# Kernel tuning notes

Measured on AMD Instinct MI355X. Metric: run time of the kernel, lower is better.

The kernel has to match this reference:

```python
import jax, jax.numpy as jnp
import numpy as np

HIDDEN = 1024
QKV = 1024
HEADS = 16
HEAD_DIM = QKV // HEADS
B, S = 4, 4096


def setup_inputs() -> dict:
    key = jax.random.key(0)
    ks = jax.random.split(key, 8)
    s = 1.0 / np.sqrt(HIDDEN)
    return {
        "x": jax.random.normal(ks[0], (B, S, HIDDEN), dtype=jnp.float32),
        "mask": jnp.ones((B, S, 1), dtype=jnp.float32),
        "Wq": jax.random.uniform(ks[1], (HIDDEN, QKV), jnp.float32, -s, s),
        "bq": jax.random.uniform(ks[2], (QKV,), jnp.float32, -s, s),
        "Wk": jax.random.uniform(ks[3], (HIDDEN, QKV), jnp.float32, -s, s),
        "bk": jax.random.uniform(ks[4], (QKV,), jnp.float32, -s, s),
        "Wv": jax.random.uniform(ks[5], (HIDDEN, QKV), jnp.float32, -s, s),
        "bv": jax.random.uniform(ks[6], (QKV,), jnp.float32, -s, s),
    }


def _split_heads(t):
    # [B, S, QKV] -> [B, H, S, D]
    b, s, _ = t.shape
    return t.reshape(b, s, HEADS, HEAD_DIM).transpose(0, 2, 1, 3)


def reference(x, mask, Wq, bq, Wk, bk, Wv, bv):
    q = (x @ Wq + bq) * mask  # [B, S, QKV]
    k = (x @ Wk + bk) * mask
    v = (x @ Wv + bv) * mask
    q, k, v = _split_heads(q), _split_heads(k), _split_heads(v)  # [B,H,S,D]
    # k^T @ v : [B, H, D, D]
    kv = jnp.einsum('bhsd,bhse->bhde', k, v)
    # per-batch norm constant from mask sum
    norm = mask.sum(axis=(-1, -2))  # [B]
    norm = 1.0 / jnp.sqrt(norm * HEAD_DIM)
    kv = kv * norm[:, None, None, None]
    # dropout is identity in eval mode
    out = jnp.einsum('bhsd,bhde->bhse', q, kv)  # [B, H, S, D]
    out = out.transpose(0, 2, 1, 3).reshape(B, S, QKV)
    return out
```

## Files before the change

kernel.cpp:

```cpp
#include <hip/hip_runtime.h>
#include <stdint.h>

#define HIDDEN 1024
#define SEQ 4096
#define BATCH 4
#define HEADS 16
#define HDIM 64
#define M_TOT (BATCH * SEQ)
#define NCH 4
#define NT64 16

typedef __bf16 bf16x8 __attribute__((ext_vector_type(8)));
typedef float f32x4 __attribute__((ext_vector_type(4)));
typedef unsigned short u16x8 __attribute__((ext_vector_type(8)));

static __device__ __forceinline__ unsigned short f2bf(float f) {
  union { float f; uint32_t u; } v; v.f = f;
  uint32_t u = v.u;
  uint32_t r = (u + 0x7fffu + ((u >> 16) & 1u)) >> 16;
  return (unsigned short)r;
}
static __device__ __forceinline__ void load_lds16(const void* g, void* l) {
  __builtin_amdgcn_global_load_lds(
      (__attribute__((address_space(1))) void*)(g),
      (__attribute__((address_space(3))) void*)(l), 16, 0, 0);
}

__global__ __launch_bounds__(256) void prep_k(
    const float* __restrict__ x, unsigned short* __restrict__ xb,
    const float* __restrict__ Wk, const float* __restrict__ Wv,
    const float* __restrict__ Wq,
    unsigned short* __restrict__ Bt, unsigned short* __restrict__ Wqt,
    const float* __restrict__ bk, const float* __restrict__ bv,
    float* __restrict__ bkv,
    const float* __restrict__ mask, float* __restrict__ norm) {
  const int bid = blockIdx.x;
  const int tid = threadIdx.x;
  __shared__ float ts[64][65];
  if (bid < 8192) {
    int idx = bid * 256 + tid;
    const float4* xv = (const float4*)x;
    float4 a = xv[(size_t)idx * 2];
    float4 b = xv[(size_t)idx * 2 + 1];
    u16x8 o;
    o[0] = f2bf(a.x); o[1] = f2bf(a.y); o[2] = f2bf(a.z); o[3] = f2bf(a.w);
    o[4] = f2bf(b.x); o[5] = f2bf(b.y); o[6] = f2bf(b.z); o[7] = f2bf(b.w);
    *(u16x8*)(xb + (size_t)idx * 8) = o;
  } else if (bid < 8960) {
    int idx = bid - 8192;
    int z = idx >> 8, rem = idx & 255;
    const float* W = (z == 0) ? Wk : (z == 1) ? Wv : Wq;
    unsigned short* out = (z == 2) ? Wqt : (Bt + (size_t)z * HIDDEN * HIDDEN);
    int n0 = (rem & 15) * 64, k0 = (rem >> 4) * 64;
    int c = tid & 63, rq = tid >> 6;
    for (int i = 0; i < 16; ++i) {
      int r = i * 4 + rq;
      ts[r][c] = W[(size_t)(k0 + r) * HIDDEN + n0 + c];
    }
    __syncthreads();
    for (int i = 0; i < 16; ++i) {
      int n = i * 4 + rq;
      out[(size_t)(n0 + n) * HIDDEN + k0 + c] = f2bf(ts[c][n]);
    }
  } else if (bid < 8968) {
    int i = (bid - 8960) * 256 + tid;
    bkv[i] = (i < HIDDEN) ? bk[i] : bv[i - HIDDEN];
  } else {
    int b = bid - 8968;
    float s = 0.f;
    for (int i = tid; i < SEQ; i += 256) s += mask[b * SEQ + i];
    for (int off = 32; off; off >>= 1) s += __shfl_down(s, off);
    __shared__ float wsum[4];
    if ((tid & 63) == 0) wsum[tid >> 6] = s;
    __syncthreads();
    if (tid == 0) {
      float t = wsum[0] + wsum[1] + wsum[2] + wsum[3];
      norm[b] = rsqrtf(t * (float)HDIM);
    }
  }
}

template <int OUT_MODE>
__global__ __launch_bounds__(512, 2) void gemm256_k(
    const unsigned short* __restrict__ A, const unsigned short* __restrict__ Bt,
    const float* __restrict__ bias, const float* __restrict__ mask,
    void* __restrict__ C, int nbn) {
  __shared__ unsigned short smem[65536];

  const int nwg = gridDim.x;
  const int bid = blockIdx.x;
  const int wg = (bid & 7) * (nwg >> 3) + (bid >> 3);
  const int row0 = (wg / nbn) * 256;
  const int col0 = (wg % nbn) * 256;

  const int tid = threadIdx.x;
  const int wave = tid >> 6;
  const int lane = tid & 63;
  const int wm = wave >> 2;
  const int wn = wave & 3;
  const int lr = lane & 15;
  const int hi = lane >> 4;

  const int srow = tid >> 3;
  const int scol = ((tid & 7) ^ (srow & 7)) * 8;
  const unsigned short* sA = A + (size_t)(row0 + srow) * HIDDEN + scol;
  const unsigned short* sB = Bt + (size_t)(col0 + srow) * HIDDEN + scol;
  const int ldst = tid * 8;

#define STAGE(half, tt, isB) { \
    int dst_ = ((tt)&1) * 32768 + (isB) * 16384 + (half) * 8192 + ldst; \
    const unsigned short* src_ = ((isB) ? sB : sA) + (size_t)(half) * 128 * HIDDEN + (tt) * 64; \
    load_lds16(src_, &smem[dst_]); \
    load_lds16(src_ + (size_t)64 * HIDDEN, &smem[dst_ + 4096]); }

  const int chunk0 = (hi ^ (lr & 7)) * 8;
  const int chunk1 = ((4 + hi) ^ (lr & 7)) * 8;
  const int arow = (wm * 128 + lr) * 64;
  const int brow = 16384 + (wn * 64 + lr) * 64;

  f32x4 acc[8][4];
#pragma unroll
  for (int i = 0; i < 8; ++i)
#pragma unroll
    for (int j = 0; j < 4; ++j) acc[i][j] = (f32x4){0.f, 0.f, 0.f, 0.f};

  STAGE(0, 0, 0) STAGE(1, 0, 0) STAGE(0, 0, 1) STAGE(1, 0, 1)
  STAGE(0, 1, 1) STAGE(1, 1, 1)
  asm volatile("s_waitcnt vmcnt(4)" ::: "memory");
  __builtin_amdgcn_s_barrier();

  bf16x8 af[4][2], b0f[2][2], b1f[2][2];
  for (int t = 0; t < NT64; ++t) {
    const int bb = (t & 1) * 32768;
#pragma unroll
    for (int rf = 0; rf < 4; ++rf) {
      af[rf][0] = *(const bf16x8*)&smem[bb + arow + rf * 1024 + chunk0];
      af[rf][1] = *(const bf16x8*)&smem[bb + arow + rf * 1024 + chunk1];
    }
#pragma unroll
    for (int cf = 0; cf < 2; ++cf) {
      b0f[cf][0] = *(const bf16x8*)&smem[bb + brow + cf * 1024 + chunk0];
      b0f[cf][1] = *(const bf16x8*)&smem[bb + brow + cf * 1024 + chunk1];
    }
    if (t + 1 < NT64) STAGE(0, t + 1, 0)
    __builtin_amdgcn_s_setprio(1);
#pragma unroll
    for (int rf = 0; rf < 4; ++rf)
#pragma unroll
      for (int cf = 0; cf < 2; ++cf)
#pragma unroll
        for (int kh = 0; kh < 2; ++kh)
          acc[rf][cf] = __builtin_amdgcn_mfma_f32_16x16x32_bf16(af[rf][kh], b0f[cf][kh], acc[rf][cf], 0, 0, 0);
    __builtin_amdgcn_s_setprio(0);
    asm volatile("" ::: "memory");
    __builtin_amdgcn_s_barrier();
#pragma unroll
    for (int cf = 0; cf < 2; ++cf) {
      b1f[cf][0] = *(const bf16x8*)&smem[bb + brow + 2048 + cf * 1024 + chunk0];
      b1f[cf][1] = *(const bf16x8*)&smem[bb + brow + 2048 + cf * 1024 + chunk1];
    }
    if (t + 1 < NT64) STAGE(1, t + 1, 0)
    __builtin_amdgcn_s_setprio(1);
#pragma unroll
    for (int rf = 0; rf < 4; ++rf)
#pragma unroll
      for (int cf = 0; cf < 2; ++cf)
#pragma unroll
        for (int kh = 0; kh < 2; ++kh)
          acc[rf][2 + cf] = __builtin_amdgcn_mfma_f32_16x16x32_bf16(af[rf][kh], b1f[cf][kh], acc[rf][2 + cf], 0, 0, 0);
    __builtin_amdgcn_s_setprio(0);
    asm volatile("" ::: "memory");
    __builtin_amdgcn_s_barrier();
#pragma unroll
    for (int rf = 0; rf < 4; ++rf) {
      af[rf][0] = *(const bf16x8*)&smem[bb + arow + 4096 + rf * 1024 + chunk0];
      af[rf][1] = *(const bf16x8*)&smem[bb + arow + 4096 + rf * 1024 + chunk1];
    }
    __builtin_amdgcn_s_setprio(1);
#pragma unroll
    for (int rf = 0; rf < 4; ++rf)
#pragma unroll
      for (int cf = 0; cf < 2; ++cf)
#pragma unroll
        for (int kh = 0; kh < 2; ++kh)
          acc[4 + rf][cf] = __builtin_amdgcn_mfma_f32_16x16x32_bf16(af[rf][kh], b0f[cf][kh], acc[4 + rf][cf], 0, 0, 0);
    __builtin_amdgcn_s_setprio(0);
    asm volatile("" ::: "memory");
    __builtin_amdgcn_s_barrier();
    if (t + 2 < NT64) { STAGE(0, t + 2, 1) STAGE(1, t + 2, 1) }
    __builtin_amdgcn_s_setprio(1);
#pragma unroll
    for (int rf = 0; rf < 4; ++rf)
#pragma unroll
      for (int cf = 0; cf < 2; ++cf)
#pragma unroll
        for (int kh = 0; kh < 2; ++kh)
          acc[4 + rf][2 + cf] = __builtin_amdgcn_mfma_f32_16x16x32_bf16(af[rf][kh], b1f[cf][kh], acc[4 + rf][2 + cf], 0, 0, 0);
    __builtin_amdgcn_s_setprio(0);
    if (t < NT64 - 3) asm volatile("s_waitcnt vmcnt(4)" ::: "memory");
    else              asm volatile("s_waitcnt vmcnt(0)" ::: "memory");
    __builtin_amdgcn_s_barrier();
  }

  float bcol[4];
#pragma unroll
  for (int an = 0; an < 4; ++an)
    bcol[an] = bias[col0 + wn * 64 + (an >> 1) * 32 + (an & 1) * 16 + lr];

  if (OUT_MODE == 2) {
    const int b = row0 >> 12;
    const int s0 = (row0 & 4095) + wm * 128;
    unsigned short* wt = &smem[wave * 4096];
    unsigned short* KVt = (unsigned short*)C;
#pragma unroll
    for (int half = 0; half < 2; ++half) {
#pragma unroll
      for (int am4 = 0; am4 < 4; ++am4) {
#pragma unroll
        for (int j = 0; j < 4; ++j) {
          int r = am4 * 16 + hi * 4 + j;
          float mrow = mask[row0 + wm * 128 + half * 64 + r];
#pragma unroll
          for (int an = 0; an < 4; ++an) {
            int c = (an >> 1) * 32 + (an & 1) * 16 + lr;
            wt[c * 64 + (r ^ ((c & 7) << 3))] =
                f2bf((acc[half * 4 + am4][an][j] + bcol[an]) * mrow);
          }
        }
      }
      asm volatile("s_waitcnt lgkmcnt(0)" ::: "memory");
#pragma unroll
      for (int i = 0; i < 8; ++i) {
        int flat = i * 64 + lane;
        int c = flat >> 3, rq = flat & 7;
        uint4 vv = *(const uint4*)&wt[c * 64 + ((rq * 8) ^ ((c & 7) << 3))];
        *(uint4*)&KVt[((size_t)(col0 + wn * 64 + c) * 4 + b) * 4096 + s0 + half * 64 + rq * 8] = vv;
      }
      asm volatile("s_waitcnt lgkmcnt(0)" ::: "memory");
    }
  } else {
    unsigned short* qv = (unsigned short*)C;
    unsigned short* wt = &smem[wave * 4096];
#pragma unroll
    for (int half = 0; half < 2; ++half) {
#pragma unroll
      for (int am4 = 0; am4 < 4; ++am4) {
#pragma unroll
        for (int j = 0; j < 4; ++j) {
          int r = am4 * 16 + hi * 4 + j;
          float mrow = mask[row0 + wm * 128 + half * 64 + r];
#pragma unroll
          for (int an = 0; an < 4; ++an) {
            int c = (an >> 1) * 32 + (an & 1) * 16 + lr;
            wt[r * 64 + (c ^ ((r & 7) << 3))] =
                f2bf((acc[half * 4 + am4][an][j] + bcol[an]) * mrow);
          }
        }
      }
      asm volatile("s_waitcnt lgkmcnt(0)" ::: "memory");
#pragma unroll
      for (int i = 0; i < 8; ++i) {
        int flat = i * 512 + lane * 8;
        int r = flat >> 6, c0 = flat & 63;
        uint4 vv = *(const uint4*)&wt[r * 64 + (c0 ^ ((r & 7) << 3))];
        *(uint4*)&qv[(size_t)(row0 + wm * 128 + half * 64 + r) * 1024 + col0 + wn * 64 + c0] = vv;
      }
      asm volatile("s_waitcnt lgkmcnt(0)" ::: "memory");
    }
  }
#undef STAGE
}

__global__ __launch_bounds__(256) void kvpart2_k(const unsigned short* __restrict__ KVt,
                                                 float* __restrict__ part) {
  const int bh = blockIdx.x, ch = blockIdx.y;
  const int b = bh >> 4, h = bh & 15;
  __shared__ unsigned short tl[32768];
  const int tid = threadIdx.x;
  const int wave = tid >> 6, lane = tid & 63;
  const int lr = lane & 15, hi = lane >> 4;

  const int r0 = tid >> 3;
  const int cc0 = ((tid & 7) ^ (r0 & 7)) * 8;
  const int r1 = 32 + r0;
  const int cc1 = ((tid & 7) ^ (r1 & 7)) * 8;
  const unsigned short* A0 = KVt + ((size_t)(h * 64 + r0) * 4 + b) * 4096 + ch * 1024 + cc0;
  const unsigned short* A1 = KVt + ((size_t)(h * 64 + r1) * 4 + b) * 4096 + ch * 1024 + cc1;
  const unsigned short* B0 = KVt + ((size_t)(1024 + h * 64 + r0) * 4 + b) * 4096 + ch * 1024 + cc0;
  const unsigned short* B1 = KVt + ((size_t)(1024 + h * 64 + r1) * 4 + b) * 4096 + ch * 1024 + cc1;

#define KSTAGE(tt) { int bb2 = ((tt) & 3) * 8192; \
    load_lds16(A0 + (tt) * 64, &tl[bb2 + tid * 8]); \
    load_lds16(A1 + (tt) * 64, &tl[bb2 + 2048 + tid * 8]); \
    load_lds16(B0 + (tt) * 64, &tl[bb2 + 4096 + tid * 8]); \
    load_lds16(B1 + (tt) * 64, &tl[bb2 + 6144 + tid * 8]); }

  const int ra = wave * 16 + lr;
  const int aoff = ra * 64;
  const int ach0 = (hi ^ (ra & 7)) * 8, ach1 = ((4 + hi) ^ (ra & 7)) * 8;

  f32x4 acc4[4];
#pragma unroll
  for (int nt = 0; nt < 4; ++nt) acc4[nt] = (f32x4){0.f, 0.f, 0.f, 0.f};

  KSTAGE(0) KSTAGE(1)
  asm volatile("s_waitcnt vmcnt(4)" ::: "memory");
  __builtin_amdgcn_s_barrier();
  for (int t = 0; t < 16; ++t) {
    const int bb = (t & 3) * 8192;
    if (t + 2 < 16) KSTAGE(t + 2)
    bf16x8 a0 = *(const bf16x8*)&tl[bb + aoff + ach0];
    bf16x8 a1 = *(const bf16x8*)&tl[bb + aoff + ach1];
    bf16x8 bf0[4], bf1[4];
#pragma unroll
    for (int nt = 0; nt < 4; ++nt) {
      int rb = nt * 16 + lr;
      bf0[nt] = *(const bf16x8*)&tl[bb + 4096 + rb * 64 + ((hi ^ (rb & 7)) * 8)];
      bf1[nt] = *(const bf16x8*)&tl[bb + 4096 + rb * 64 + (((4 + hi) ^ (rb & 7)) * 8)];
    }
#pragma unroll
    for (int nt = 0; nt < 4; ++nt) {
      acc4[nt] = __builtin_amdgcn_mfma_f32_16x16x32_bf16(a0, bf0[nt], acc4[nt], 0, 0, 0);
      acc4[nt] = __builtin_amdgcn_mfma_f32_16x16x32_bf16(a1, bf1[nt], acc4[nt], 0, 0, 0);
    }
    if (t < 14) asm volatile("s_waitcnt vmcnt(4)" ::: "memory");
    else        asm volatile("s_waitcnt vmcnt(0)" ::: "memory");
    __builtin_amdgcn_s_barrier();
  }
  float* dst = part + ((size_t)(ch * 64 + bh)) * 4096;
#pragma unroll
  for (int nt = 0; nt < 4; ++nt)
#pragma unroll
    for (int j = 0; j < 4; ++j)
      dst[(wave * 16 + hi * 4 + j) * 64 + nt * 16 + lr] = acc4[nt][j];
#undef KSTAGE
}

__global__ void kvreduce_k(const float* __restrict__ part, const float* __restrict__ norm,
                           unsigned short* __restrict__ kvt) {
  int idx4 = (blockIdx.x * 256 + threadIdx.x) * 4;
  int bh = idx4 >> 12, rem = idx4 & 4095;
  int e = rem >> 6, d0 = rem & 63;
  float s0 = 0.f, s1 = 0.f, s2 = 0.f, s3 = 0.f;
#pragma unroll
  for (int ch = 0; ch < NCH; ++ch) {
    const float* p = part + ((size_t)(ch * 64 + bh)) * 4096 + e;
    s0 += p[(d0 + 0) * 64];
    s1 += p[(d0 + 1) * 64];
    s2 += p[(d0 + 2) * 64];
    s3 += p[(d0 + 3) * 64];
  }
  float nb = norm[bh >> 4];
  ushort4 o;
  o.x = f2bf(s0 * nb); o.y = f2bf(s1 * nb); o.z = f2bf(s2 * nb); o.w = f2bf(s3 * nb);
  *(ushort4*)&kvt[idx4] = o;
}

__global__ __launch_bounds__(256) void qkv_k(const unsigned short* __restrict__ q,
                                             const unsigned short* __restrict__ kvt,
                                             float* __restrict__ out) {
  const int s0 = blockIdx.x * 64;
  const int b = s0 >> 12;
  const int tid = threadIdx.x;
  const int wave = tid >> 6, lane = tid & 63;
  const int lr = lane & 15, hi = lane >> 4;
  const unsigned short* qrow = q + (size_t)(s0 + wave * 16 + lr) * 1024;
#pragma unroll 1
  for (int h = 0; h < 16; ++h) {
    const unsigned short* kvb = kvt + ((size_t)(b * 16 + h)) * 4096;
    bf16x8 a0 = *(const bf16x8*)&qrow[h * 64 + hi * 8];
    bf16x8 a1 = *(const bf16x8*)&qrow[h * 64 + 32 + hi * 8];
    f32x4 acc4[4];
#pragma unroll
    for (int et = 0; et < 4; ++et) {
      bf16x8 b0 = *(const bf16x8*)&kvb[(et * 16 + lr) * 64 + hi * 8];
      bf16x8 b1 = *(const bf16x8*)&kvb[(et * 16 + lr) * 64 + 32 + hi * 8];
      acc4[et] = (f32x4){0.f, 0.f, 0.f, 0.f};
      acc4[et] = __builtin_amdgcn_mfma_f32_16x16x32_bf16(a0, b0, acc4[et], 0, 0, 0);
      acc4[et] = __builtin_amdgcn_mfma_f32_16x16x32_bf16(a1, b1, acc4[et], 0, 0, 0);
    }
#pragma unroll
    for (int et = 0; et < 4; ++et)
#pragma unroll
      for (int j = 0; j < 4; ++j)
        __builtin_nontemporal_store(acc4[et][j],
            &out[(size_t)(s0 + wave * 16 + hi * 4 + j) * 1024 + h * 64 + et * 16 + lr]);
  }
}

extern "C" void kernel_launch(void* const* d_in, const int* in_sizes, int n_in,
                              void* d_out, int out_size, void* d_ws, size_t ws_size,
                              hipStream_t stream) {
  const float* x = (const float*)d_in[0];
  const float* mask = (const float*)d_in[1];
  const float* Wq = (const float*)d_in[2];
  const float* bq = (const float*)d_in[3];
  const float* Wk = (const float*)d_in[4];
  const float* bk = (const float*)d_in[5];
  const float* Wv = (const float*)d_in[6];
  const float* bv = (const float*)d_in[7];
  float* out = (float*)d_out;

  char* w = (char*)d_ws;
  unsigned short* xb = (unsigned short*)w;   w += (size_t)M_TOT * HIDDEN * 2;
  unsigned short* Bt = (unsigned short*)w;   w += (size_t)2048 * HIDDEN * 2;
  unsigned short* Wqt = (unsigned short*)w;  w += (size_t)HIDDEN * HIDDEN * 2;
  unsigned short* KVt = (unsigned short*)w;  w += (size_t)2048 * BATCH * SEQ * 2;
  float* part = (float*)w;                   w += (size_t)NCH * 64 * 4096 * 4;
  unsigned short* kvt = (unsigned short*)w;  w += (size_t)64 * 4096 * 2;
  float* bkv = (float*)w;                    w += 2048 * 4;
  float* norm = (float*)w;                   w += 64;
  unsigned short* q = KVt;

  prep_k<<<dim3(8972), dim3(256), 0, stream>>>(x, xb, Wk, Wv, Wq, Bt, Wqt, bk, bv, bkv, mask, norm);
  gemm256_k<2><<<dim3(512), dim3(512), 0, stream>>>(xb, Bt, bkv, mask, (void*)KVt, 8);
  kvpart2_k<<<dim3(64, NCH), dim3(256), 0, stream>>>(KVt, part);
  kvreduce_k<<<dim3(256), dim3(256), 0, stream>>>(part, norm, kvt);
  gemm256_k<3><<<dim3(256), dim3(512), 0, stream>>>(xb, Wqt, bq, mask, (void*)q, 4);
  qkv_k<<<dim3(256), dim3(256), 0, stream>>>(q, kvt, out);
}
```

Baseline: 168.9 us.

## Fuse Q-times-KV product into the Q projection GEMM epilogue

The Q projection GEMM epilogue now keeps each 64-column head tile in LDS as bf16 and multiplies it by the per-head KV matrix with MFMA, writing fp32 output directly. This removes the separate qkv_k kernel and the round trip of the bf16 Q tensor through global memory. It adds register pressure (KV fragments plus output accumulators) to an already heavy GEMM epilogue. The template argument changes to 4, and chunk0/chunk1 are used without being visible in the diff, so correctness depends on unseen code.

Result: faster. 154.4 us, median of 2 (-8.6%).

```diff
diff --git a/kernel.cpp b/kernel.cpp
--- a/kernel.cpp
+++ b/kernel.cpp
@@ -84,6 +84,7 @@
 __global__ __launch_bounds__(512, 2) void gemm256_k(
     const unsigned short* __restrict__ A, const unsigned short* __restrict__ Bt,
     const float* __restrict__ bias, const float* __restrict__ mask,
+    const unsigned short* __restrict__ kvt,
     void* __restrict__ C, int nbn) {
   __shared__ unsigned short smem[65536];
 
@@ -239,8 +240,16 @@
       asm volatile("s_waitcnt lgkmcnt(0)" ::: "memory");
     }
   } else {
-    unsigned short* qv = (unsigned short*)C;
+    float* Og = (float*)C;
+    const int b = row0 >> 12;
+    const int bh = b * 16 + (col0 >> 6) + wn;
     unsigned short* wt = &smem[wave * 4096];
+    bf16x8 kvf[4][2];
+#pragma unroll
+    for (int et = 0; et < 4; ++et) {
+      kvf[et][0] = *(const bf16x8*)&kvt[(size_t)bh * 4096 + (et * 16 + lr) * 64 + hi * 8];
+      kvf[et][1] = *(const bf16x8*)&kvt[(size_t)bh * 4096 + (et * 16 + lr) * 64 + 32 + hi * 8];
+    }
 #pragma unroll
     for (int half = 0; half < 2; ++half) {
 #pragma unroll
@@ -258,13 +267,27 @@
         }
       }
       asm volatile("s_waitcnt lgkmcnt(0)" ::: "memory");
-#pragma unroll
-      for (int i = 0; i < 8; ++i) {
-        int flat = i * 512 + lane * 8;
-        int r = flat >> 6, c0 = flat & 63;
-        uint4 vv = *(const uint4*)&wt[r * 64 + (c0 ^ ((r & 7) << 3))];
-        *(uint4*)&qv[(size_t)(row0 + wm * 128 + half * 64 + r) * 1024 + col0 + wn * 64 + c0] = vv;
+      f32x4 oacc[4][4];
+#pragma unroll
+      for (int g = 0; g < 4; ++g) {
+        bf16x8 a0 = *(const bf16x8*)&wt[(g * 16 + lr) * 64 + chunk0];
+        bf16x8 a1 = *(const bf16x8*)&wt[(g * 16 + lr) * 64 + chunk1];
+#pragma unroll
+        for (int et = 0; et < 4; ++et) {
+          oacc[g][et] = (f32x4){0.f, 0.f, 0.f, 0.f};
+          oacc[g][et] = __builtin_amdgcn_mfma_f32_16x16x32_bf16(a0, kvf[et][0], oacc[g][et], 0, 0, 0);
+          oacc[g][et] = __builtin_amdgcn_mfma_f32_16x16x32_bf16(a1, kvf[et][1], oacc[g][et], 0, 0, 0);
+        }
       }
+#pragma unroll
+      for (int g = 0; g < 4; ++g)
+#pragma unroll
+        for (int et = 0; et < 4; ++et)
+#pragma unroll
+          for (int j = 0; j < 4; ++j)
+            __builtin_nontemporal_store(oacc[g][et][j],
+                &Og[(size_t)(row0 + wm * 128 + half * 64 + g * 16 + hi * 4 + j) * 1024
+                    + col0 + wn * 64 + et * 16 + lr]);
       asm volatile("s_waitcnt lgkmcnt(0)" ::: "memory");
     }
   }
@@ -354,38 +377,6 @@
   ushort4 o;
   o.x = f2bf(s0 * nb); o.y = f2bf(s1 * nb); o.z = f2bf(s2 * nb); o.w = f2bf(s3 * nb);
   *(ushort4*)&kvt[idx4] = o;
-}
-
-__global__ __launch_bounds__(256) void qkv_k(const unsigned short* __restrict__ q,
-                                             const unsigned short* __restrict__ kvt,
-                                             float* __restrict__ out) {
-  const int s0 = blockIdx.x * 64;
-  const int b = s0 >> 12;
-  const int tid = threadIdx.x;
-  const int wave = tid >> 6, lane = tid & 63;
-  const int lr = lane & 15, hi = lane >> 4;
-  const unsigned short* qrow = q + (size_t)(s0 + wave * 16 + lr) * 1024;
-#pragma unroll 1
-  for (int h = 0; h < 16; ++h) {
-    const unsigned short* kvb = kvt + ((size_t)(b * 16 + h)) * 4096;
-    bf16x8 a0 = *(const bf16x8*)&qrow[h * 64 + hi * 8];
-    bf16x8 a1 = *(const bf16x8*)&qrow[h * 64 + 32 + hi * 8];
-    f32x4 acc4[4];
-#pragma unroll
-    for (int et = 0; et < 4; ++et) {
-      bf16x8 b0 = *(const bf16x8*)&kvb[(et * 16 + lr) * 64 + hi * 8];
-      bf16x8 b1 = *(const bf16x8*)&kvb[(et * 16 + lr) * 64 + 32 + hi * 8];
-      acc4[et] = (f32x4){0.f, 0.f, 0.f, 0.f};
-      acc4[et] = __builtin_amdgcn_mfma_f32_16x16x32_bf16(a0, b0, acc4[et], 0, 0, 0);
-      acc4[et] = __builtin_amdgcn_mfma_f32_16x16x32_bf16(a1, b1, acc4[et], 0, 0, 0);
-    }
-#pragma unroll
-    for (int et = 0; et < 4; ++et)
-#pragma unroll
-      for (int j = 0; j < 4; ++j)
-        __builtin_nontemporal_store(acc4[et][j],
-            &out[(size_t)(s0 + wave * 16 + hi * 4 + j) * 1024 + h * 64 + et * 16 + lr]);
-  }
 }
 
 extern "C" void kernel_launch(void* const* d_in, const int* in_sizes, int n_in,
@@ -410,12 +401,10 @@
   unsigned short* kvt = (unsigned short*)w;  w += (size_t)64 * 4096 * 2;
   float* bkv = (float*)w;                    w += 2048 * 4;
   float* norm = (float*)w;                   w += 64;
-  unsigned short* q = KVt;
 
   prep_k<<<dim3(8972), dim3(256), 0, stream>>>(x, xb, Wk, Wv, Wq, Bt, Wqt, bk, bv, bkv, mask, norm);
-  gemm256_k<2><<<dim3(512), dim3(512), 0, stream>>>(xb, Bt, bkv, mask, (void*)KVt, 8);
+  gemm256_k<2><<<dim3(512), dim3(512), 0, stream>>>(xb, Bt, bkv, mask, nullptr, (void*)KVt, 8);
   kvpart2_k<<<dim3(64, NCH), dim3(256), 0, stream>>>(KVt, part);
   kvreduce_k<<<dim3(256), dim3(256), 0, stream>>>(part, norm, kvt);
-  gemm256_k<3><<<dim3(256), dim3(512), 0, stream>>>(xb, Wqt, bq, mask, (void*)q, 4);
-  qkv_k<<<dim3(256), dim3(256), 0, stream>>>(q, kvt, out);
-}
+  gemm256_k<4><<<dim3(256), dim3(512), 0, stream>>>(xb, Wqt, bq, mask, kvt, (void*)out, 4);
+}
```
